# Performance work log

Hardware: AMD Instinct MI355X
Metric: run time of the kernel (lower is better)

Reference implementation:

```python
import jax, jax.numpy as jnp
import numpy as np

TEMPERATURE = 0.5
NEG_INF_FILL = -1000000000.0


def setup_inputs() -> dict:
    key = jax.random.key(0)
    z = jax.random.normal(key, (16384, 128), dtype=jnp.float32)
    # module expects L2-normalized projected features
    z = z / jnp.linalg.norm(z, axis=-1, keepdims=True)
    return {"z": z}


def reference(z) -> jnp.ndarray:
    N2 = z.shape[0]
    N = N2 // 2
    # (2N, 2N) pairwise similarity scaled by temperature
    sim = (z @ z.T) / TEMPERATURE
    # mask self-similarity on the diagonal
    eye = jnp.eye(N2, dtype=bool)
    sim = jnp.where(eye, NEG_INF_FILL, sim)
    # positive pair index: row i < N pairs with i+N; row i >= N pairs with i-N
    pos_idx = jnp.concatenate([jnp.arange(N, N2), jnp.arange(0, N)])
    positives = sim[jnp.arange(N2), pos_idx]
    loss = -positives + jax.scipy.special.logsumexp(sim, axis=1)
    return loss.mean()
```

## Files before the change

kernel.cpp:

```cpp
#include <hip/hip_runtime.h>
#include <hip/hip_bf16.h>

#define N2    16384
#define NHALF 8192
#define KDIM  128
#define BROW  128
#define BCOL  128
#define NQUARTER 4096
#define NITER (NQUARTER / BCOL)

using bf16x8 = __attribute__((ext_vector_type(8))) short;
using f32x4  = __attribute__((ext_vector_type(4))) float;

#if __has_builtin(__builtin_amdgcn_exp2f)
#define EXP2F(x) __builtin_amdgcn_exp2f(x)
#else
#define EXP2F(x) exp2f(x)
#endif
#if __has_builtin(__builtin_amdgcn_logf)
#define LOG2F(x) __builtin_amdgcn_logf(x)
#else
#define LOG2F(x) log2f(x)
#endif

#define PRESCALE 1.6986436005760381f

typedef const __attribute__((address_space(1))) void* gas_ptr;
typedef __attribute__((address_space(3))) void* las_ptr;

__device__ __forceinline__ unsigned short f2bf(float f) {
  unsigned u = __float_as_uint(f);
  u += 0x7fffu + ((u >> 16) & 1u);
  return (unsigned short)(u >> 16);
}

__global__ void k_convert(const float* __restrict__ z, unsigned short* __restrict__ zb,
                          float* __restrict__ S, float* __restrict__ out) {
  int i = blockIdx.x * blockDim.x + threadIdx.x;
  if (i < N2) S[i] = 0.f;
  if (i == 0) out[0] = 0.f;
  float4 v = reinterpret_cast<const float4*>(z)[i];
  ushort4 o;
  o.x = f2bf(v.x * PRESCALE); o.y = f2bf(v.y * PRESCALE);
  o.z = f2bf(v.z * PRESCALE); o.w = f2bf(v.w * PRESCALE);
  reinterpret_cast<ushort4*>(zb)[i] = o;
}

__global__ __launch_bounds__(512, 2) void k_main(const unsigned short* __restrict__ zb,
                                                 float* __restrict__ S) {
  __shared__ __align__(16) unsigned short Bs[2][BCOL * KDIM];
  const int t    = threadIdx.x;
  const int w    = t >> 6;
  const int l    = t & 63;
  const int q    = l >> 4;
  const int c15  = l & 15;
  const int bt      = blockIdx.x >> 2;
  const int quarter = blockIdx.x & 3;
  const int mg   = w >> 2;
  const int ns   = w & 3;
  const int rbase = bt * BROW + mg * 64;

  int srcoff[4];
#pragma unroll
  for (int j = 0; j < 4; ++j) {
    int p   = (w * 4 + j) * 64 + l;
    int row = p >> 4;
    int pg  = p & 15;
    int k8  = pg ^ (row & 15);
    srcoff[j] = (row * 16 + k8) * 16;
  }

  const char* tile0 = (const char*)zb + (size_t)(quarter * NQUARTER) * KDIM * 2;

#pragma unroll
  for (int j = 0; j < 4; ++j)
    __builtin_amdgcn_global_load_lds((gas_ptr)(tile0 + srcoff[j]),
                                     (las_ptr)(&Bs[0][(w * 4 + j) * 512]), 16, 0, 0);

  bf16x8 afr[4][4];
#pragma unroll
  for (int m = 0; m < 4; ++m) {
    const unsigned short* ap = zb + (size_t)(rbase + m * 16 + c15) * KDIM + q * 8;
#pragma unroll
    for (int s = 0; s < 4; ++s)
      afr[m][s] = *reinterpret_cast<const bf16x8*>(ap + s * 32);
  }

  float rowsum[4][4];
#pragma unroll
  for (int m = 0; m < 4; ++m)
#pragma unroll
    for (int r = 0; r < 4; ++r) rowsum[m][r] = 0.f;

  for (int it = 0; it < NITER; ++it) {
    const int buf = it & 1;
    const int C0  = quarter * NQUARTER + it * BCOL;
    __syncthreads();

    if (it + 1 < NITER) {
      const char* src = tile0 + (size_t)(it + 1) * BCOL * KDIM * 2;
#pragma unroll
      for (int j = 0; j < 4; ++j)
        __builtin_amdgcn_global_load_lds((gas_ptr)(src + srcoff[j]),
                                         (las_ptr)(&Bs[buf ^ 1][(w * 4 + j) * 512]), 16, 0, 0);
    }

    bf16x8 bfr[4][2];
#pragma unroll
    for (int s = 0; s < 4; ++s)
#pragma unroll
      for (int n = 0; n < 2; ++n) {
        int rloc = ns * 32 + n * 16 + c15;
        int pg   = (s * 4 + q) ^ (rloc & 15);
        bfr[s][n] = *reinterpret_cast<const bf16x8*>(&Bs[buf][rloc * KDIM + pg * 8]);
      }

    const int dOff = (C0 + ns * 32) - rbase;

#pragma unroll
    for (int m = 0; m < 4; ++m)
#pragma unroll
      for (int n = 0; n < 2; ++n) {
        f32x4 acc = (f32x4){0.f, 0.f, 0.f, 0.f};
#pragma unroll
        for (int s = 0; s < 4; ++s)
          acc = __builtin_amdgcn_mfma_f32_16x16x32_bf16(afr[m][s], bfr[s][n], acc, 0, 0, 0);
        const bool dfrag = (dOff == (m - n) * 16);
#pragma unroll
        for (int r = 0; r < 4; ++r) {
          float e = EXP2F(acc[r]);
          if (dfrag && (c15 == q * 4 + r)) e = 0.f;
          rowsum[m][r] += e;
        }
      }
  }

#pragma unroll
  for (int m = 0; m < 4; ++m)
#pragma unroll
    for (int r = 0; r < 4; ++r) {
      float v = rowsum[m][r];
      v += __shfl_xor(v, 1);
      v += __shfl_xor(v, 2);
      v += __shfl_xor(v, 4);
      v += __shfl_xor(v, 8);
      if (c15 == 0) atomicAdd(&S[rbase + m * 16 + q * 4 + r], v);
    }
}

__global__ void k_final(const float* __restrict__ z, const float* __restrict__ S,
                        float* __restrict__ out) {
  __shared__ float red[256];
  int t = threadIdx.x;
  int i = blockIdx.x * 256 + t;
  int j = i ^ NHALF;
  const float4* zi = reinterpret_cast<const float4*>(z + (size_t)i * KDIM);
  const float4* zj = reinterpret_cast<const float4*>(z + (size_t)j * KDIM);
  float dot = 0.f;
#pragma unroll
  for (int k = 0; k < KDIM / 4; ++k) {
    float4 a = zi[k], b = zj[k];
    dot += a.x * b.x + a.y * b.y + a.z * b.z + a.w * b.w;
  }
  float loss = LOG2F(S[i]) * 0.69314718055994531f - 2.f * dot;
  red[t] = loss;
  __syncthreads();
  for (int o = 128; o > 0; o >>= 1) {
    if (t < o) red[t] += red[t + o];
    __syncthreads();
  }
  if (t == 0) atomicAdd(out, red[0] * (1.f / N2));
}

extern "C" void kernel_launch(void* const* d_in, const int* in_sizes, int n_in,
                              void* d_out, int out_size, void* d_ws, size_t ws_size,
                              hipStream_t stream) {
  const float* z = (const float*)d_in[0];
  float* out = (float*)d_out;
  unsigned short* zb = (unsigned short*)d_ws;
  float* S = (float*)((char*)d_ws + (size_t)N2 * KDIM * 2);

  k_convert<<<(N2 * KDIM / 4) / 256, 256, 0, stream>>>(z, zb, S, out);
  k_main<<<512, 512, 0, stream>>>(zb, S);
  k_final<<<N2 / 256, 256, 0, stream>>>(z, S, out);
}
```

Before: 146.6 us.

## Drop LDS staging and load B fragments directly from global memory

Removes the shared-memory double-buffered B tile and its barriers. Each wave now reads its B fragments straight from global memory (L2/L1) into registers. Blocks shrink to 256 threads covering 64 rows, with four times as many blocks and higher occupancy. This removes LDS traffic and sync overhead, but each wave now reloads B independently, so global and cache traffic rise and load latency is no longer overlapped by explicit prefetch.

```diff
diff --git a/kernel.cpp b/kernel.cpp
--- a/kernel.cpp
+++ b/kernel.cpp
@@ -4,7 +4,6 @@
 #define N2    16384
 #define NHALF 8192
 #define KDIM  128
-#define BROW  128
 #define BCOL  128
 #define NQUARTER 4096
 #define NITER (NQUARTER / BCOL)
@@ -25,9 +24,6 @@
 
 #define PRESCALE 1.6986436005760381f
 
-typedef const __attribute__((address_space(1))) void* gas_ptr;
-typedef __attribute__((address_space(3))) void* las_ptr;
-
 __device__ __forceinline__ unsigned short f2bf(float f) {
   unsigned u = __float_as_uint(f);
   u += 0x7fffu + ((u >> 16) & 1u);
@@ -46,36 +42,16 @@
   reinterpret_cast<ushort4*>(zb)[i] = o;
 }
 
-__global__ __launch_bounds__(512, 2) void k_main(const unsigned short* __restrict__ zb,
+__global__ __launch_bounds__(256, 4) void k_main(const unsigned short* __restrict__ zb,
                                                  float* __restrict__ S) {
-  __shared__ __align__(16) unsigned short Bs[2][BCOL * KDIM];
   const int t    = threadIdx.x;
   const int w    = t >> 6;
   const int l    = t & 63;
   const int q    = l >> 4;
   const int c15  = l & 15;
-  const int bt      = blockIdx.x >> 2;
+  const int rg      = blockIdx.x >> 2;
   const int quarter = blockIdx.x & 3;
-  const int mg   = w >> 2;
-  const int ns   = w & 3;
-  const int rbase = bt * BROW + mg * 64;
-
-  int srcoff[4];
-#pragma unroll
-  for (int j = 0; j < 4; ++j) {
-    int p   = (w * 4 + j) * 64 + l;
-    int row = p >> 4;
-    int pg  = p & 15;
-    int k8  = pg ^ (row & 15);
-    srcoff[j] = (row * 16 + k8) * 16;
-  }
-
-  const char* tile0 = (const char*)zb + (size_t)(quarter * NQUARTER) * KDIM * 2;
-
-#pragma unroll
-  for (int j = 0; j < 4; ++j)
-    __builtin_amdgcn_global_load_lds((gas_ptr)(tile0 + srcoff[j]),
-                                     (las_ptr)(&Bs[0][(w * 4 + j) * 512]), 16, 0, 0);
+  const int rbase = rg * 64;
 
   bf16x8 afr[4][4];
 #pragma unroll
@@ -92,30 +68,17 @@
 #pragma unroll
     for (int r = 0; r < 4; ++r) rowsum[m][r] = 0.f;
 
+  const unsigned short* bp =
+      zb + (size_t)(quarter * NQUARTER + w * 32 + c15) * KDIM + q * 8;
+  int dOff = (quarter * NQUARTER + w * 32) - rbase;
+
   for (int it = 0; it < NITER; ++it) {
-    const int buf = it & 1;
-    const int C0  = quarter * NQUARTER + it * BCOL;
-    __syncthreads();
-
-    if (it + 1 < NITER) {
-      const char* src = tile0 + (size_t)(it + 1) * BCOL * KDIM * 2;
-#pragma unroll
-      for (int j = 0; j < 4; ++j)
-        __builtin_amdgcn_global_load_lds((gas_ptr)(src + srcoff[j]),
-                                         (las_ptr)(&Bs[buf ^ 1][(w * 4 + j) * 512]), 16, 0, 0);
-    }
-
     bf16x8 bfr[4][2];
 #pragma unroll
-    for (int s = 0; s < 4; ++s)
+    for (int n = 0; n < 2; ++n)
 #pragma unroll
-      for (int n = 0; n < 2; ++n) {
-        int rloc = ns * 32 + n * 16 + c15;
-        int pg   = (s * 4 + q) ^ (rloc & 15);
-        bfr[s][n] = *reinterpret_cast<const bf16x8*>(&Bs[buf][rloc * KDIM + pg * 8]);
-      }
-
-    const int dOff = (C0 + ns * 32) - rbase;
+      for (int s = 0; s < 4; ++s)
+        bfr[s][n] = *reinterpret_cast<const bf16x8*>(bp + n * 16 * KDIM + s * 32);
 
 #pragma unroll
     for (int m = 0; m < 4; ++m)
@@ -133,6 +96,9 @@
           rowsum[m][r] += e;
         }
       }
+
+    bp   += (size_t)BCOL * KDIM;
+    dOff += BCOL;
   }
 
 #pragma unroll
@@ -181,6 +147,6 @@
   float* S = (float*)((char*)d_ws + (size_t)N2 * KDIM * 2);
 
   k_convert<<<(N2 * KDIM / 4) / 256, 256, 0, stream>>>(z, zb, S, out);
-  k_main<<<512, 512, 0, stream>>>(zb, S);
+  k_main<<<(N2 / 64) * 4, 256, 0, stream>>>(zb, S);
   k_final<<<N2 / 256, 256, 0, stream>>>(z, S, out);
 }
```

New measurement: 196.7 us. +34.2%, slower.
